# Kernel tuning notes

Measured on AMD Instinct MI355X. Metric: run time of the kernel, lower is better.

Reference implementation:

```python
import jax, jax.numpy as jnp
import numpy as np

N = 10000          # nodes
E = 160000         # edges (before self-loops)
F_IN = 256
H, C = 8, 64       # heads, channels per head
NUM_CLASSES = 40
NEG_SLOPE = 0.2    # PyG GATConv default leaky_relu slope


def setup_inputs() -> dict:
    key = jax.random.key(0)
    ks = jax.random.split(key, 16)
    s = 0.1  # keep logits tame
    x = jax.random.normal(ks[0], (N, F_IN), jnp.float32)
    edge_index = jax.random.randint(ks[1], (2, E), 0, N)
    W0 = jax.random.normal(ks[2], (F_IN, H * C), jnp.float32) / np.sqrt(F_IN)
    a_src0 = jax.random.normal(ks[3], (H, C), jnp.float32) * s
    a_dst0 = jax.random.normal(ks[4], (H, C), jnp.float32) * s
    b0 = jnp.zeros((H * C,), jnp.float32)
    W1 = jax.random.normal(ks[5], (H * C, H * C), jnp.float32) / np.sqrt(H * C)
    a_src1 = jax.random.normal(ks[6], (H, C), jnp.float32) * s
    a_dst1 = jax.random.normal(ks[7], (H, C), jnp.float32) * s
    b1 = jnp.zeros((H * C,), jnp.float32)
    W2 = jax.random.normal(ks[8], (H * C, NUM_CLASSES), jnp.float32) / np.sqrt(H * C)
    a_src2 = jax.random.normal(ks[9], (1, NUM_CLASSES), jnp.float32) * s
    a_dst2 = jax.random.normal(ks[10], (1, NUM_CLASSES), jnp.float32) * s
    b2 = jnp.zeros((NUM_CLASSES,), jnp.float32)
    return dict(x=x, edge_index=edge_index, W0=W0, a_src0=a_src0, a_dst0=a_dst0, b0=b0,
                W1=W1, a_src1=a_src1, a_dst1=a_dst1, b1=b1,
                W2=W2, a_src2=a_src2, a_dst2=a_dst2, b2=b2)


def gat_conv(x, src, dst, W, a_src, a_dst, b, concat):
    """PyG GATConv (eval mode: dropout = identity)."""
    n = x.shape[0]
    h, c = a_src.shape
    hx = (x @ W).reshape(n, h, c)                       # [N,H,C]
    al_s = jnp.sum(hx * a_src, axis=-1)                 # [N,H]
    al_d = jnp.sum(hx * a_dst, axis=-1)                 # [N,H]
    e = jax.nn.leaky_relu(al_s[src] + al_d[dst], NEG_SLOPE)  # [E,H]
    # neighbor softmax over incoming edges of each dst node
    m = jax.ops.segment_max(e, dst, num_segments=n)     # [N,H]
    ex = jnp.exp(e - m[dst])
    denom = jax.ops.segment_sum(ex, dst, num_segments=n)
    alpha = ex / (denom[dst] + 1e-16)                   # [E,H]
    msg = hx[src] * alpha[:, :, None]                   # [E,H,C]
    out = jax.ops.segment_sum(msg, dst, num_segments=n) # [N,H,C]
    out = out.reshape(n, h * c) if concat else out.mean(axis=1)
    return out + b


def reference(x, edge_index, W0, a_src0, a_dst0, b0, W1, a_src1, a_dst1, b1,
              W2, a_src2, a_dst2, b2):
    # add self-loops once (PyG GATConv add_self_loops=True)
    loops = jnp.arange(N, dtype=edge_index.dtype)
    src = jnp.concatenate([edge_index[0], loops])
    dst = jnp.concatenate([edge_index[1], loops])
    x = jax.nn.elu(gat_conv(x, src, dst, W0, a_src0, a_dst0, b0, True))
    x = jax.nn.elu(gat_conv(x, src, dst, W1, a_src1, a_dst1, b1, True))
    return gat_conv(x, src, dst, W2, a_src2, a_dst2, b2, False)
```

## Files before the change

### kernel.cpp

```cpp
#include <hip/hip_runtime.h>
#include <math.h>

#define NN 10000
#define EE 160000
#define ET 170000
#define FIN 256
#define HH 8
#define CC 64
#define HC 512
#define NCLS 40
#define ELLW 96

typedef unsigned short u16;
typedef unsigned int u32;
typedef _Float16 f16;
using f16x8 = __attribute__((ext_vector_type(8))) _Float16;
using f32x4 = __attribute__((ext_vector_type(4))) float;

#define MFMA16(a, b, c) __builtin_amdgcn_mfma_f32_16x16x32_f16((a), (b), (c), 0, 0, 0)

__global__ __launch_bounds__(256) void zero_int(int* p, int n) {
    int i = blockIdx.x * 256 + threadIdx.x;
    if (i < n) p[i] = 0;
}

__global__ __launch_bounds__(256) void scatter_ell(const int* __restrict__ ei,
                                                   int* __restrict__ cnt,
                                                   int* __restrict__ ell) {
    int e = blockIdx.x * 256 + threadIdx.x;
    if (e >= ET) return;
    int s, d;
    if (e < EE) { s = ei[e]; d = ei[EE + e]; }
    else        { s = e - EE; d = s; }
    int pos = atomicAdd(&cnt[d], 1);
    if (pos < ELLW) ell[(size_t)d * ELLW + pos] = s;
}

__global__ __launch_bounds__(256) void convW_kernel(const float* __restrict__ W0,
                                                    const float* __restrict__ W1,
                                                    const float* __restrict__ W2,
                                                    f16* __restrict__ w0T,
                                                    f16* __restrict__ w1T,
                                                    f16* __restrict__ w2T) {
    int i = blockIdx.x * 256 + threadIdx.x;
    if (i < HC * FIN) {
        int n = i >> 8, k = i & 255;
        w0T[i] = (f16)W0[(size_t)k * HC + n];
    } else if (i < HC * FIN + HC * HC) {
        int j = i - HC * FIN;
        int n = j >> 9, k = j & 511;
        w1T[j] = (f16)W1[(size_t)k * HC + n];
    } else if (i < HC * FIN + HC * HC + NCLS * HC) {
        int j = i - HC * FIN - HC * HC;
        int n = j >> 9, k = j & 511;
        w2T[j] = (f16)W2[(size_t)k * NCLS + n];
    }
}

template <int K, bool AF32>
__global__ __launch_bounds__(512) void gemm_attn(const void* __restrict__ Aptr,
                                                 const f16* __restrict__ BT,
                                                 const float* __restrict__ a_src,
                                                 const float* __restrict__ a_dst,
                                                 f16* __restrict__ hx2,
                                                 float* __restrict__ al_s,
                                                 float* __restrict__ al_d) {
    constexpr int KK = K / 32;
    constexpr int CH = K / 8;
    __shared__ f16 Bs[64 * K];
    int t = threadIdx.x;
    int hp = blockIdx.x;
    int lane = t & 63, w = t >> 6;
    int fm = lane & 15, g = lane >> 4;
    int bm = blockIdx.y * 128 + w * 16;
    int row = bm + fm;
    bool rok = row < NN;

    f16x8 af[KK];
    if (AF32) {
        const float* A = (const float*)Aptr;
#pragma unroll
        for (int kk = 0; kk < KK; ++kk) {
            float4 lo = make_float4(0.f, 0.f, 0.f, 0.f), hi = lo;
            if (rok) {
                const float* ap = A + (size_t)row * K + kk * 32 + g * 8;
                lo = *(const float4*)ap;
                hi = *(const float4*)(ap + 4);
            }
            f16x8 v;
            v[0] = (f16)lo.x; v[1] = (f16)lo.y; v[2] = (f16)lo.z; v[3] = (f16)lo.w;
            v[4] = (f16)hi.x; v[5] = (f16)hi.y; v[6] = (f16)hi.z; v[7] = (f16)hi.w;
            af[kk] = v;
        }
    } else {
        const f16* A = (const f16*)Aptr;
#pragma unroll
        for (int kk = 0; kk < KK; ++kk) {
            uint4 r = rok ? *(const uint4*)(A + (size_t)row * K + kk * 32 + g * 8)
                          : make_uint4(0u, 0u, 0u, 0u);
            af[kk] = __builtin_bit_cast(f16x8, r);
        }
    }

    for (int sl = 0; sl < 2; ++sl) {
        int h = hp * 2 + sl;
        const f16* bsrc = BT + (size_t)h * 64 * K;
        for (int c = t; c < 64 * CH; c += 512) {
            int brow = c / CH;
            int j = c - brow * CH;
            uint4 v = *(const uint4*)(bsrc + (size_t)brow * K + j * 8);
            *(uint4*)&Bs[(size_t)brow * K + ((j ^ (brow & 7)) * 8)] = v;
        }
        __syncthreads();

        f32x4 acc[4] = {};
#pragma unroll
        for (int kk = 0; kk < KK; ++kk) {
#pragma unroll
            for (int nt = 0; nt < 4; ++nt) {
                f16x8 b = *(const f16x8*)
                    &Bs[(nt * 16 + fm) * K + (((kk * 4 + g) ^ (fm & 7)) * 8)];
                acc[nt] = MFMA16(af[kk], b, acc[nt]);
            }
        }

        float asc[4], adc[4];
#pragma unroll
        for (int nt = 0; nt < 4; ++nt) {
            asc[nt] = a_src[h * 64 + nt * 16 + fm];
            adc[nt] = a_dst[h * 64 + nt * 16 + fm];
        }
#pragma unroll
        for (int r = 0; r < 4; ++r) {
            int orow = bm + g * 4 + r;
            float s = acc[0][r] * asc[0] + acc[1][r] * asc[1] +
                      acc[2][r] * asc[2] + acc[3][r] * asc[3];
            float d = acc[0][r] * adc[0] + acc[1][r] * adc[1] +
                      acc[2][r] * adc[2] + acc[3][r] * adc[3];
#pragma unroll
            for (int off = 1; off < 16; off <<= 1) {
                s += __shfl_xor(s, off);
                d += __shfl_xor(d, off);
            }
            if (orow < NN) {
                if (fm == 0) {
                    al_s[orow * 8 + h] = s;
                    al_d[orow * 8 + h] = d;
                }
#pragma unroll
                for (int nt = 0; nt < 4; ++nt)
                    hx2[(size_t)orow * HC + h * 64 + nt * 16 + fm] =
                        (f16)acc[nt][r];
            }
        }
        __syncthreads();
    }
}

__global__ __launch_bounds__(256) void gemm2_attn(const f16* __restrict__ A,
                                                  const f16* __restrict__ BT,
                                                  const float* __restrict__ a_src2,
                                                  const float* __restrict__ a_dst2,
                                                  float* __restrict__ hx40,
                                                  float* __restrict__ als2,
                                                  float* __restrict__ ald2) {
    __shared__ f16 As[16 * 40];
    __shared__ f16 Bs[64 * 40];
    __shared__ float pss[4][16];
    __shared__ float psd[4][16];
    int t = threadIdx.x;
    int bm = blockIdx.x * 16;
    int lane = t & 63, w = t >> 6;
    int fm = lane & 15, g = lane >> 4, ks = g * 8;

    int arow = t >> 4, akoff = (t & 15) * 2;
    bool a_ok = (bm + arow) < NN;

    f32x4 acc = {};
    u32 rah;
    uint4 rb;
    auto loadA = [&](int k0) {
        rah = a_ok ? *(const u32*)(A + (size_t)(bm + arow) * HC + k0 + akoff) : 0u;
    };
    auto loadB = [&](int k0) {
        int n = t >> 2, koff = (t & 3) * 8;
        rb = (n < NCLS) ? *(const uint4*)(BT + (size_t)n * HC + k0 + koff)
                        : make_uint4(0u, 0u, 0u, 0u);
    };
    loadA(0);
    loadB(0);
    for (int k0 = 0; k0 < HC; k0 += 32) {
        *(u32*)&As[arow * 40 + akoff] = rah;
        *(uint4*)&Bs[(t >> 2) * 40 + (t & 3) * 8] = rb;
        __syncthreads();
        if (k0 + 32 < HC) { loadA(k0 + 32); loadB(k0 + 32); }
        f16x8 a = *(const f16x8*)&As[fm * 40 + ks];
        f16x8 b = *(const f16x8*)&Bs[(w * 16 + fm) * 40 + ks];
        acc = MFMA16(a, b, acc);
        __syncthreads();
    }

    int col = w * 16 + fm;
    float a2s = (col < NCLS) ? a_src2[col] : 0.f;
    float a2d = (col < NCLS) ? a_dst2[col] : 0.f;
#pragma unroll
    for (int r = 0; r < 4; ++r) {
        int lrow = g * 4 + r;
        int row = bm + lrow;
        float s = acc[r] * a2s;
        float d = acc[r] * a2d;
#pragma unroll
        for (int off = 1; off < 16; off <<= 1) {
            s += __shfl_xor(s, off);
            d += __shfl_xor(d, off);
        }
        if (fm == 0) { pss[w][lrow] = s; psd[w][lrow] = d; }
        if (row < NN && col < NCLS) hx40[(size_t)row * NCLS + col] = acc[r];
    }
    __syncthreads();
    if (t < 16 && bm + t < NN) {
        als2[bm + t] = pss[0][t] + pss[1][t] + pss[2][t] + pss[3][t];
        ald2[bm + t] = psd[0][t] + psd[1][t] + psd[2][t] + psd[3][t];
    }
}

__global__ __launch_bounds__(256) void agg_ell(const f16* __restrict__ hx2,
                                               const float* __restrict__ al_s,
                                               const float* __restrict__ al_d,
                                               const int* __restrict__ cnt,
                                               const int* __restrict__ ell,
                                               const float* __restrict__ bias,
                                               f16* __restrict__ outF) {
    int n = blockIdx.x;
    int tid = threadIdx.x;
    int ch = tid * 2;
    int h = ch >> 6;
    float ald = al_d[n * HH + h];
    int dg = cnt[n]; if (dg > ELLW) dg = ELLW;
    const int* ep = ell + (size_t)n * ELLW;
    float a0 = 0.f, a1 = 0.f, den = 0.f;
    int i = 0;
    for (; i + 4 <= dg; i += 4) {
        int s0 = ep[i], s1 = ep[i + 1], s2 = ep[i + 2], s3 = ep[i + 3];
        float e0 = al_s[s0 * HH + h], e1 = al_s[s1 * HH + h];
        float e2 = al_s[s2 * HH + h], e3 = al_s[s3 * HH + h];
        u32 v0 = *(const u32*)(hx2 + (size_t)s0 * HC + ch);
        u32 v1 = *(const u32*)(hx2 + (size_t)s1 * HC + ch);
        u32 v2 = *(const u32*)(hx2 + (size_t)s2 * HC + ch);
        u32 v3 = *(const u32*)(hx2 + (size_t)s3 * HC + ch);
        e0 += ald; e0 = e0 > 0.f ? e0 : 0.2f * e0;
        e1 += ald; e1 = e1 > 0.f ? e1 : 0.2f * e1;
        e2 += ald; e2 = e2 > 0.f ? e2 : 0.2f * e2;
        e3 += ald; e3 = e3 > 0.f ? e3 : 0.2f * e3;
        float w0 = __expf(e0), w1 = __expf(e1), w2 = __expf(e2), w3 = __expf(e3);
        float2 f0 = make_float2((float)__builtin_bit_cast(f16, (u16)(v0 & 0xFFFF)),
                                (float)__builtin_bit_cast(f16, (u16)(v0 >> 16)));
        float2 f1 = make_float2((float)__builtin_bit_cast(f16, (u16)(v1 & 0xFFFF)),
                                (float)__builtin_bit_cast(f16, (u16)(v1 >> 16)));
        float2 f2 = make_float2((float)__builtin_bit_cast(f16, (u16)(v2 & 0xFFFF)),
                                (float)__builtin_bit_cast(f16, (u16)(v2 >> 16)));
        float2 f3 = make_float2((float)__builtin_bit_cast(f16, (u16)(v3 & 0xFFFF)),
                                (float)__builtin_bit_cast(f16, (u16)(v3 >> 16)));
        a0 += w0 * f0.x + w1 * f1.x + w2 * f2.x + w3 * f3.x;
        a1 += w0 * f0.y + w1 * f1.y + w2 * f2.y + w3 * f3.y;
        den += w0 + w1 + w2 + w3;
    }
    for (; i < dg; ++i) {
        int s = ep[i];
        float e = al_s[s * HH + h] + ald;
        e = e > 0.f ? e : 0.2f * e;
        float wgt = __expf(e);
        u32 v = *(const u32*)(hx2 + (size_t)s * HC + ch);
        a0 += wgt * (float)__builtin_bit_cast(f16, (u16)(v & 0xFFFF));
        a1 += wgt * (float)__builtin_bit_cast(f16, (u16)(v >> 16));
        den += wgt;
    }
    float inv = 1.f / (den + 1e-16f);
    float o0 = a0 * inv + bias[ch];
    float o1 = a1 * inv + bias[ch + 1];
    o0 = o0 > 0.f ? o0 : expm1f(o0);
    o1 = o1 > 0.f ? o1 : expm1f(o1);
    u32 pack = (u32)__builtin_bit_cast(u16, (f16)o0) |
               ((u32)__builtin_bit_cast(u16, (f16)o1) << 16);
    *(u32*)(outF + (size_t)n * HC + ch) = pack;
}

__global__ __launch_bounds__(64) void agg2_final(const float* __restrict__ hx40,
                                                 const float* __restrict__ als,
                                                 const float* __restrict__ aldp,
                                                 const int* __restrict__ cnt,
                                                 const int* __restrict__ ell,
                                                 const float* __restrict__ b2,
                                                 float* __restrict__ out) {
    int n = blockIdx.x;
    int c = threadIdx.x;
    float ald = aldp[n];
    int dg = cnt[n]; if (dg > ELLW) dg = ELLW;
    const int* ep = ell + (size_t)n * ELLW;
    float acc = 0.f, den = 0.f;
    int i = 0;
    for (; i + 4 <= dg; i += 4) {
        int s0 = ep[i], s1 = ep[i + 1], s2 = ep[i + 2], s3 = ep[i + 3];
        float e0 = als[s0], e1 = als[s1], e2 = als[s2], e3 = als[s3];
        float v0 = 0.f, v1 = 0.f, v2 = 0.f, v3 = 0.f;
        if (c < NCLS) {
            v0 = hx40[(size_t)s0 * NCLS + c];
            v1 = hx40[(size_t)s1 * NCLS + c];
            v2 = hx40[(size_t)s2 * NCLS + c];
            v3 = hx40[(size_t)s3 * NCLS + c];
        }
        e0 += ald; e0 = e0 > 0.f ? e0 : 0.2f * e0;
        e1 += ald; e1 = e1 > 0.f ? e1 : 0.2f * e1;
        e2 += ald; e2 = e2 > 0.f ? e2 : 0.2f * e2;
        e3 += ald; e3 = e3 > 0.f ? e3 : 0.2f * e3;
        float w0 = __expf(e0), w1 = __expf(e1), w2 = __expf(e2), w3 = __expf(e3);
        acc += w0 * v0 + w1 * v1 + w2 * v2 + w3 * v3;
        den += w0 + w1 + w2 + w3;
    }
    for (; i < dg; ++i) {
        int s = ep[i];
        float e = als[s] + ald;
        e = e > 0.f ? e : 0.2f * e;
        float wgt = __expf(e);
        if (c < NCLS) acc += wgt * hx40[(size_t)s * NCLS + c];
        den += wgt;
    }
    if (c < NCLS) out[(size_t)n * NCLS + c] = acc / (den + 1e-16f) + b2[c];
}

extern "C" void kernel_launch(void* const* d_in, const int* in_sizes, int n_in,
                              void* d_out, int out_size, void* d_ws, size_t ws_size,
                              hipStream_t stream) {
    const float* x   = (const float*)d_in[0];
    const int*   ei  = (const int*)  d_in[1];
    const float* W0  = (const float*)d_in[2];
    const float* as0 = (const float*)d_in[3];
    const float* ad0 = (const float*)d_in[4];
    const float* b0  = (const float*)d_in[5];
    const float* W1  = (const float*)d_in[6];
    const float* as1 = (const float*)d_in[7];
    const float* ad1 = (const float*)d_in[8];
    const float* b1  = (const float*)d_in[9];
    const float* W2  = (const float*)d_in[10];
    const float* as2 = (const float*)d_in[11];
    const float* ad2 = (const float*)d_in[12];
    const float* b2  = (const float*)d_in[13];
    float* out = (float*)d_out;

    char* p = (char*)d_ws;
    int* cnt  = (int*)p; p += 40064;
    int* ell  = (int*)p; p += (size_t)NN * ELLW * 4;
    f16* w0T  = (f16*)p; p += HC * FIN * 2;
    f16* w1T  = (f16*)p; p += HC * HC * 2;
    f16* w2T  = (f16*)p; p += NCLS * HC * 2;
    f16* hxA  = (f16*)p; p += (size_t)NN * HC * 2;
    f16* hxB  = (f16*)p; p += (size_t)NN * HC * 2;
    f16* fA   = (f16*)p; p += (size_t)NN * HC * 2;
    f16* fB   = (f16*)p; p += (size_t)NN * HC * 2;
    float* hx40 = (float*)p; p += (size_t)NN * NCLS * 4;
    float* als0 = (float*)p; p += NN * HH * 4;
    float* ald0 = (float*)p; p += NN * HH * 4;
    float* als1 = (float*)p; p += NN * HH * 4;
    float* ald1 = (float*)p; p += NN * HH * 4;
    float* als2 = (float*)p; p += NN * 4;
    float* ald2 = (float*)p; p += NN * 4;

    const int NBR = (NN + 127) / 128;
    const int NB2 = (NN + 15) / 16;

    zero_int<<<(NN + 255) / 256, 256, 0, stream>>>(cnt, NN);
    scatter_ell<<<(ET + 255) / 256, 256, 0, stream>>>(ei, cnt, ell);
    convW_kernel<<<(HC * FIN + HC * HC + NCLS * HC + 255) / 256, 256, 0, stream>>>(
        W0, W1, W2, w0T, w1T, w2T);

    dim3 gA(4, NBR);
    gemm_attn<FIN, true><<<gA, 512, 0, stream>>>(x, w0T, as0, ad0, hxA, als0, ald0);
    agg_ell<<<NN, 256, 0, stream>>>(hxA, als0, ald0, cnt, ell, b0, fA);
    gemm_attn<HC, false><<<gA, 512, 0, stream>>>(fA, w1T, as1, ad1, hxB, als1, ald1);
    agg_ell<<<NN, 256, 0, stream>>>(hxB, als1, ald1, cnt, ell, b1, fB);
    gemm2_attn<<<NB2, 256, 0, stream>>>(fB, w2T, as2, ad2, hx40, als2, ald2);
    agg2_final<<<NN, 64, 0, stream>>>(hx40, als2, ald2, cnt, ell, b2, out);
}
```

Measured before the change: 216.7 us.

## Vectorize aggregation to one wave per node and restructure final GEMM tiling

```diff
diff --git a/kernel.cpp b/kernel.cpp
--- a/kernel.cpp
+++ b/kernel.cpp
@@ -164,63 +164,66 @@
                                                   float* __restrict__ hx40,
                                                   float* __restrict__ als2,
                                                   float* __restrict__ ald2) {
-    __shared__ f16 As[16 * 40];
-    __shared__ f16 Bs[64 * 40];
-    __shared__ float pss[4][16];
-    __shared__ float psd[4][16];
+    __shared__ f16 Bs[48 * HC];
     int t = threadIdx.x;
-    int bm = blockIdx.x * 16;
     int lane = t & 63, w = t >> 6;
-    int fm = lane & 15, g = lane >> 4, ks = g * 8;
-
-    int arow = t >> 4, akoff = (t & 15) * 2;
-    bool a_ok = (bm + arow) < NN;
-
-    f32x4 acc = {};
-    u32 rah;
-    uint4 rb;
-    auto loadA = [&](int k0) {
-        rah = a_ok ? *(const u32*)(A + (size_t)(bm + arow) * HC + k0 + akoff) : 0u;
-    };
-    auto loadB = [&](int k0) {
-        int n = t >> 2, koff = (t & 3) * 8;
-        rb = (n < NCLS) ? *(const uint4*)(BT + (size_t)n * HC + k0 + koff)
-                        : make_uint4(0u, 0u, 0u, 0u);
-    };
-    loadA(0);
-    loadB(0);
-    for (int k0 = 0; k0 < HC; k0 += 32) {
-        *(u32*)&As[arow * 40 + akoff] = rah;
-        *(uint4*)&Bs[(t >> 2) * 40 + (t & 3) * 8] = rb;
-        __syncthreads();
-        if (k0 + 32 < HC) { loadA(k0 + 32); loadB(k0 + 32); }
-        f16x8 a = *(const f16x8*)&As[fm * 40 + ks];
-        f16x8 b = *(const f16x8*)&Bs[(w * 16 + fm) * 40 + ks];
-        acc = MFMA16(a, b, acc);
-        __syncthreads();
-    }
-
-    int col = w * 16 + fm;
-    float a2s = (col < NCLS) ? a_src2[col] : 0.f;
-    float a2d = (col < NCLS) ? a_dst2[col] : 0.f;
+    int fm = lane & 15, g = lane >> 4;
+    int bm = blockIdx.x * 64 + w * 16;
+    int row = bm + fm;
+    bool rok = row < NN;
+
+    for (int c = t; c < 48 * 64; c += 256) {
+        int brow = c >> 6, j = c & 63;
+        uint4 v = make_uint4(0u, 0u, 0u, 0u);
+        if (brow < NCLS) v = *(const uint4*)(BT + (size_t)brow * HC + j * 8);
+        *(uint4*)&Bs[brow * HC + ((j ^ (brow & 7)) * 8)] = v;
+    }
+
+    f16x8 af[16];
+#pragma unroll
+    for (int kk = 0; kk < 16; ++kk) {
+        uint4 r = rok ? *(const uint4*)(A + (size_t)row * HC + kk * 32 + g * 8)
+                      : make_uint4(0u, 0u, 0u, 0u);
+        af[kk] = __builtin_bit_cast(f16x8, r);
+    }
+    __syncthreads();
+
+    f32x4 acc[3] = {};
+#pragma unroll
+    for (int kk = 0; kk < 16; ++kk) {
+#pragma unroll
+        for (int nt = 0; nt < 3; ++nt) {
+            f16x8 b = *(const f16x8*)
+                &Bs[(nt * 16 + fm) * HC + (((kk * 4 + g) ^ (fm & 7)) * 8)];
+            acc[nt] = MFMA16(af[kk], b, acc[nt]);
+        }
+    }
+
+    float a2s[3], a2d[3];
+#pragma unroll
+    for (int nt = 0; nt < 3; ++nt) {
+        int col = nt * 16 + fm;
+        a2s[nt] = (col < NCLS) ? a_src2[col] : 0.f;
+        a2d[nt] = (col < NCLS) ? a_dst2[col] : 0.f;
+    }
 #pragma unroll
     for (int r = 0; r < 4; ++r) {
-        int lrow = g * 4 + r;
-        int row = bm + lrow;
-        float s = acc[r] * a2s;
-        float d = acc[r] * a2d;
+        int orow = bm + g * 4 + r;
+        float s = acc[0][r] * a2s[0] + acc[1][r] * a2s[1] + acc[2][r] * a2s[2];
+        float d = acc[0][r] * a2d[0] + acc[1][r] * a2d[1] + acc[2][r] * a2d[2];
 #pragma unroll
         for (int off = 1; off < 16; off <<= 1) {
             s += __shfl_xor(s, off);
             d += __shfl_xor(d, off);
         }
-        if (fm == 0) { pss[w][lrow] = s; psd[w][lrow] = d; }
-        if (row < NN && col < NCLS) hx40[(size_t)row * NCLS + col] = acc[r];
-    }
-    __syncthreads();
-    if (t < 16 && bm + t < NN) {
-        als2[bm + t] = pss[0][t] + pss[1][t] + pss[2][t] + pss[3][t];
-        ald2[bm + t] = psd[0][t] + psd[1][t] + psd[2][t] + psd[3][t];
+        if (orow < NN) {
+            if (fm == 0) { als2[orow] = s; ald2[orow] = d; }
+#pragma unroll
+            for (int nt = 0; nt < 3; ++nt) {
+                int col = nt * 16 + fm;
+                if (col < NCLS) hx40[(size_t)orow * NCLS + col] = acc[nt][r];
+            }
+        }
     }
 }
 
@@ -231,38 +234,38 @@
                                                const int* __restrict__ ell,
                                                const float* __restrict__ bias,
                                                f16* __restrict__ outF) {
-    int n = blockIdx.x;
-    int tid = threadIdx.x;
-    int ch = tid * 2;
-    int h = ch >> 6;
+    int lane = threadIdx.x & 63, w = threadIdx.x >> 6;
+    int n = blockIdx.x * 4 + w;
+    if (n >= NN) return;
+    int ch = lane * 8;
+    int h = lane >> 3;
     float ald = al_d[n * HH + h];
     int dg = cnt[n]; if (dg > ELLW) dg = ELLW;
     const int* ep = ell + (size_t)n * ELLW;
-    float a0 = 0.f, a1 = 0.f, den = 0.f;
+    float acc[8] = {0.f, 0.f, 0.f, 0.f, 0.f, 0.f, 0.f, 0.f};
+    float den = 0.f;
     int i = 0;
     for (; i + 4 <= dg; i += 4) {
         int s0 = ep[i], s1 = ep[i + 1], s2 = ep[i + 2], s3 = ep[i + 3];
         float e0 = al_s[s0 * HH + h], e1 = al_s[s1 * HH + h];
         float e2 = al_s[s2 * HH + h], e3 = al_s[s3 * HH + h];
-        u32 v0 = *(const u32*)(hx2 + (size_t)s0 * HC + ch);
-        u32 v1 = *(const u32*)(hx2 + (size_t)s1 * HC + ch);
-        u32 v2 = *(const u32*)(hx2 + (size_t)s2 * HC + ch);
-        u32 v3 = *(const u32*)(hx2 + (size_t)s3 * HC + ch);
+        uint4 v0 = *(const uint4*)(hx2 + (size_t)s0 * HC + ch);
+        uint4 v1 = *(const uint4*)(hx2 + (size_t)s1 * HC + ch);
+        uint4 v2 = *(const uint4*)(hx2 + (size_t)s2 * HC + ch);
+        uint4 v3 = *(const uint4*)(hx2 + (size_t)s3 * HC + ch);
         e0 += ald; e0 = e0 > 0.f ? e0 : 0.2f * e0;
         e1 += ald; e1 = e1 > 0.f ? e1 : 0.2f * e1;
         e2 += ald; e2 = e2 > 0.f ? e2 : 0.2f * e2;
         e3 += ald; e3 = e3 > 0.f ? e3 : 0.2f * e3;
         float w0 = __expf(e0), w1 = __expf(e1), w2 = __expf(e2), w3 = __expf(e3);
-        float2 f0 = make_float2((float)__builtin_bit_cast(f16, (u16)(v0 & 0xFFFF)),
-                                (float)__builtin_bit_cast(f16, (u16)(v0 >> 16)));
-        float2 f1 = make_float2((float)__builtin_bit_cast(f16, (u16)(v1 & 0xFFFF)),
-                                (float)__builtin_bit_cast(f16, (u16)(v1 >> 16)));
-        float2 f2 = make_float2((float)__builtin_bit_cast(f16, (u16)(v2 & 0xFFFF)),
-                                (float)__builtin_bit_cast(f16, (u16)(v2 >> 16)));
-        float2 f3 = make_float2((float)__builtin_bit_cast(f16, (u16)(v3 & 0xFFFF)),
-                                (float)__builtin_bit_cast(f16, (u16)(v3 >> 16)));
-        a0 += w0 * f0.x + w1 * f1.x + w2 * f2.x + w3 * f3.x;
-        a1 += w0 * f0.y + w1 * f1.y + w2 * f2.y + w3 * f3.y;
+        f16x8 f0 = __builtin_bit_cast(f16x8, v0);
+        f16x8 f1 = __builtin_bit_cast(f16x8, v1);
+        f16x8 f2 = __builtin_bit_cast(f16x8, v2);
+        f16x8 f3 = __builtin_bit_cast(f16x8, v3);
+#pragma unroll
+        for (int j = 0; j < 8; ++j)
+            acc[j] += w0 * (float)f0[j] + w1 * (float)f1[j] +
+                      w2 * (float)f2[j] + w3 * (float)f3[j];
         den += w0 + w1 + w2 + w3;
     }
     for (; i < dg; ++i) {
@@ -270,19 +273,24 @@
         float e = al_s[s * HH + h] + ald;
         e = e > 0.f ? e : 0.2f * e;
         float wgt = __expf(e);
-        u32 v = *(const u32*)(hx2 + (size_t)s * HC + ch);
-        a0 += wgt * (float)__builtin_bit_cast(f16, (u16)(v & 0xFFFF));
-        a1 += wgt * (float)__builtin_bit_cast(f16, (u16)(v >> 16));
+        uint4 v = *(const uint4*)(hx2 + (size_t)s * HC + ch);
+        f16x8 f = __builtin_bit_cast(f16x8, v);
+#pragma unroll
+        for (int j = 0; j < 8; ++j) acc[j] += wgt * (float)f[j];
         den += wgt;
     }
     float inv = 1.f / (den + 1e-16f);
-    float o0 = a0 * inv + bias[ch];
-    float o1 = a1 * inv + bias[ch + 1];
-    o0 = o0 > 0.f ? o0 : expm1f(o0);
-    o1 = o1 > 0.f ? o1 : expm1f(o1);
-    u32 pack = (u32)__builtin_bit_cast(u16, (f16)o0) |
-               ((u32)__builtin_bit_cast(u16, (f16)o1) << 16);
-    *(u32*)(outF + (size_t)n * HC + ch) = pack;
+    float4 b0v = *(const float4*)(bias + ch);
+    float4 b1v = *(const float4*)(bias + ch + 4);
+    float bb[8] = {b0v.x, b0v.y, b0v.z, b0v.w, b1v.x, b1v.y, b1v.z, b1v.w};
+    f16x8 o;
+#pragma unroll
+    for (int j = 0; j < 8; ++j) {
+        float v = acc[j] * inv + bb[j];
+        v = v > 0.f ? v : expm1f(v);
+        o[j] = (f16)v;
+    }
+    *(uint4*)(outF + (size_t)n * HC + ch) = __builtin_bit_cast(uint4, o);
 }
 
 __global__ __launch_bounds__(64) void agg2_final(const float* __restrict__ hx40,
@@ -366,7 +374,8 @@
     float* ald2 = (float*)p; p += NN * 4;
 
     const int NBR = (NN + 127) / 128;
-    const int NB2 = (NN + 15) / 16;
+    const int NAG = (NN + 3) / 4;
+    const int NB2 = (NN + 63) / 64;
 
     zero_int<<<(NN + 255) / 256, 256, 0, stream>>>(cnt, NN);
     scatter_ell<<<(ET + 255) / 256, 256, 0, stream>>>(ei, cnt, ell);
@@ -375,9 +384,9 @@
 
     dim3 gA(4, NBR);
     gemm_attn<FIN, true><<<gA, 512, 0, stream>>>(x, w0T, as0, ad0, hxA, als0, ald0);
-    agg_ell<<<NN, 256, 0, stream>>>(hxA, als0, ald0, cnt, ell, b0, fA);
+    agg_ell<<<NAG, 256, 0, stream>>>(hxA, als0, ald0, cnt, ell, b0, fA);
     gemm_attn<HC, false><<<gA, 512, 0, stream>>>(fA, w1T, as1, ad1, hxB, als1, ald1);
-    agg_ell<<<NN, 256, 0, stream>>>(hxB, als1, ald1, cnt, ell, b1, fB);
+    agg_ell<<<NAG, 256, 0, stream>>>(hxB, als1, ald1, cnt, ell, b1, fB);
     gemm2_attn<<<NB2, 256, 0, stream>>>(fB, w2T, as2, ad2, hx40, als2, ald2);
     agg2_final<<<NN, 64, 0, stream>>>(hx40, als2, ald2, cnt, ell, b2, out);
 }
```

New measurement: 207.5 us. 1.04x faster.
